# Kernel tuning notes

Hardware: AMD Instinct MI355X
Metric: run time of the kernel (lower is better)

Reference implementation:

```python
import jax, jax.numpy as jnp
import numpy as np
from math import comb

N_SEG = 100000      # number of Bezier segments
BEZ_ORDER = 3       # cubic Bezier -> 4 control points per segment
D = 3               # point dimension
BATCH, NPTS = 8, 1000000


def setup_inputs() -> dict:
    key = jax.random.key(0)
    k1, k2, k3 = jax.random.split(key, 3)
    # strictly ascending knot vector: cumsum of positive dx, starting at 0
    dx = jax.random.uniform(k1, (N_SEG,), dtype=jnp.float32, minval=0.5, maxval=1.5)
    x_knots = jnp.concatenate([jnp.zeros((1,), jnp.float32), jnp.cumsum(dx)])
    x_end = x_knots[-1]
    # eval points spread beyond [0, x_end) so the modulo wrap is exercised
    x_eval = jax.random.uniform(k2, (BATCH, NPTS), dtype=jnp.float32) * (2.0 * x_end) - 0.5 * x_end
    control_points = jax.random.normal(k3, (N_SEG, BEZ_ORDER + 1, D), dtype=jnp.float32)
    return {"x_knots": x_knots, "control_points": control_points, "x_eval": x_eval}


def _bernstein_basis(s, n):
    # s: [N] in [0,1] -> basis [N, n+1]; powers via cumprod (differentiable at s=0/1)
    binom = jnp.asarray([comb(n, k) for k in range(n + 1)], dtype=s.dtype)
    t = s[:, None]
    ones = jnp.ones_like(t)
    t_pow = jnp.cumprod(jnp.concatenate([ones, jnp.broadcast_to(t, (t.shape[0], n))], axis=1), axis=1)         # t^k
    u = 1.0 - t
    u_pow = jnp.cumprod(jnp.concatenate([ones, jnp.broadcast_to(u, (u.shape[0], n))], axis=1), axis=1)         # u^k
    return binom * t_pow * u_pow[:, ::-1]  # C(n,k) t^k (1-t)^(n-k)


def reference(x_knots, control_points, x_eval):
    n = control_points.shape[1] - 1
    d = control_points.shape[2]
    xstart = x_knots[:-1]                      # [n_seg]
    dx = x_knots[1:] - x_knots[:-1]            # [n_seg]
    # x_true = x_eval % xend  (Python modulo semantics, matches torch %)
    x_true = jnp.mod(x_eval.reshape(-1), x_knots[-1])        # [N]
    # bucket search: segment index such that xstart[i] <= x_true < xstart[i+1]
    idx = jnp.clip(jnp.searchsorted(xstart, x_true, side='right') - 1, 0, xstart.shape[0] - 1)
    s = (x_true - xstart[idx]) / dx[idx]                     # local param in [0,1)
    basis = _bernstein_basis(s, n)                           # [N, n+1]
    P = control_points[idx]                                  # gather: [N, n+1, d]
    vals = jnp.einsum('nk,nkd->nd', basis, P)                # [N, d]
    return vals.reshape(x_eval.shape + (d,)), idx.reshape(x_eval.shape)
```

## Files before the change

kernel.cpp:

```cpp
#include <hip/hip_runtime.h>
#include <hip/hip_fp16.h>
#include <math.h>

#define N_SEG 100000
#define LUT_BITS 18
#define LUT_SIZE (1 << LUT_BITS)
#define DELTA 0.03

using f32x4 = __attribute__((ext_vector_type(4))) float;

#define LUT_OFF 0
#define REC_OFF 2097152
#define WS_NEED (REC_OFF + (size_t)N_SEG * 32)

__global__ void __launch_bounds__(256)
build_lut_kernel(const float* __restrict__ xk, int2* __restrict__ lut) {
    int j = blockIdx.x * blockDim.x + threadIdx.x;
    if (j >= LUT_SIZE) return;
    double Wd = (double)xk[N_SEG] / (double)LUT_SIZE;
    double t = (double)j * Wd - DELTA;
    int lo = 0, hi = N_SEG;
    while (lo < hi) {
        int mid = (lo + hi) >> 1;
        if ((double)xk[mid] <= t) lo = mid + 1; else hi = mid;
    }
    int base = lo - 1;
    base = base < 0 ? 0 : (base > N_SEG - 1 ? N_SEG - 1 : base);
    int2 e;
    e.x = base;
    e.y = (base + 1 <= N_SEG - 1) ? __float_as_int(xk[base + 1])
                                  : __float_as_int(__builtin_inff());
    lut[j] = e;
}

__device__ __forceinline__ unsigned packh(float lo, float hi) {
    unsigned a = (unsigned)__half_as_ushort(__float2half(lo));
    unsigned b = (unsigned)__half_as_ushort(__float2half(hi));
    return a | (b << 16);
}

__global__ void __launch_bounds__(256)
build_rec_kernel(const float* __restrict__ xk, const float* __restrict__ cp,
                 uint4* __restrict__ rec) {
    int i = blockIdx.x * blockDim.x + threadIdx.x;
    if (i >= N_SEG) return;
    float x0 = xk[i];
    float inv = 1.0f / (xk[i + 1] - x0);
    const f32x4* p = reinterpret_cast<const f32x4*>(cp + (size_t)i * 12);
    f32x4 pA = p[0];
    f32x4 pB = p[1];
    f32x4 pC = p[2];
    uint4 ra, rb;
    ra.x = __float_as_uint(x0);
    ra.y = __float_as_uint(inv);
    ra.z = packh(pA.x, pA.y);
    ra.w = packh(pA.z, pA.w);
    rb.x = packh(pB.x, pB.y);
    rb.y = packh(pB.z, pB.w);
    rb.z = packh(pC.x, pC.y);
    rb.w = packh(pC.z, pC.w);
    rec[2 * (size_t)i]     = ra;
    rec[2 * (size_t)i + 1] = rb;
}

__device__ __forceinline__ float h2f(unsigned w, int hi) {
    return __half2float(__ushort_as_half((unsigned short)(hi ? (w >> 16) : (w & 0xFFFFu))));
}

__device__ __forceinline__ float mod_reduce(float x, float xe) {
    float r = x;
    r = (x >= xe) ? (x - xe) : r;
    r = (x < 0.0f) ? (x + xe) : r;
    return r;
}

__global__ void __launch_bounds__(256, 4)
eval_kernel(const float* __restrict__ xk,
            const float* __restrict__ xev,
            float* __restrict__ out_vals,
            float* __restrict__ out_idx,
            const int2* __restrict__ lut,
            const uint4* __restrict__ rec,
            int npts) {
    int t = blockIdx.x * blockDim.x + threadIdx.x;
    int i0 = t * 8;
    if (i0 >= npts) return;

    float xe = xk[N_SEG];
    float invW = (float)LUT_SIZE / xe;

    if (i0 + 7 < npts) {
        f32x4 xa = __builtin_nontemporal_load(reinterpret_cast<const f32x4*>(xev) + 2 * t);
        f32x4 xb = __builtin_nontemporal_load(reinterpret_cast<const f32x4*>(xev) + 2 * t + 1);
        float r[8] = {xa.x, xa.y, xa.z, xa.w, xb.x, xb.y, xb.z, xb.w};
        int2 e[8];
        #pragma unroll
        for (int q = 0; q < 8; ++q) {
            r[q] = mod_reduce(r[q], xe);
            int j = (int)(r[q] * invW);
            j = j < 0 ? 0 : (j > LUT_SIZE - 1 ? LUT_SIZE - 1 : j);
            e[q] = lut[j];
        }
        int idx[8];
        uint4 ra[8], rb[8];
        #pragma unroll
        for (int q = 0; q < 8; ++q) {
            idx[q] = e[q].x + ((__int_as_float(e[q].y) <= r[q]) ? 1 : 0);
            ra[q] = rec[2 * (size_t)idx[q]];
            rb[q] = rec[2 * (size_t)idx[q] + 1];
        }
        float vals[24];
        float idxf[8];
        #pragma unroll
        for (int q = 0; q < 8; ++q) {
            float x0  = __uint_as_float(ra[q].x);
            float inv = __uint_as_float(ra[q].y);
            float s = (r[q] - x0) * inv;
            float u = 1.0f - s;
            float s2 = s * s, u2 = u * u;
            float b0 = u2 * u;
            float b1 = (3.0f * s) * u2;
            float b2 = (3.0f * s2) * u;
            float b3 = s2 * s;
            float c0 = h2f(ra[q].z, 0), c1  = h2f(ra[q].z, 1);
            float c2 = h2f(ra[q].w, 0), c3  = h2f(ra[q].w, 1);
            float c4 = h2f(rb[q].x, 0), c5  = h2f(rb[q].x, 1);
            float c6 = h2f(rb[q].y, 0), c7  = h2f(rb[q].y, 1);
            float c8 = h2f(rb[q].z, 0), c9  = h2f(rb[q].z, 1);
            float c10 = h2f(rb[q].w, 0), c11 = h2f(rb[q].w, 1);
            vals[q * 3 + 0] = b0 * c0 + b1 * c3 + b2 * c6 + b3 * c9;
            vals[q * 3 + 1] = b0 * c1 + b1 * c4 + b2 * c7 + b3 * c10;
            vals[q * 3 + 2] = b0 * c2 + b1 * c5 + b2 * c8 + b3 * c11;
            idxf[q] = (float)idx[q];
        }
        f32x4* ov = reinterpret_cast<f32x4*>(out_vals + (size_t)t * 24);
        #pragma unroll
        for (int q = 0; q < 6; ++q) {
            f32x4 o = {vals[4 * q], vals[4 * q + 1], vals[4 * q + 2], vals[4 * q + 3]};
            ov[q] = o;
        }
        f32x4 oi0 = {idxf[0], idxf[1], idxf[2], idxf[3]};
        f32x4 oi1 = {idxf[4], idxf[5], idxf[6], idxf[7]};
        reinterpret_cast<f32x4*>(out_idx)[2 * t]     = oi0;
        reinterpret_cast<f32x4*>(out_idx)[2 * t + 1] = oi1;
    } else {
        for (int i = i0; i < npts; ++i) {
            float r = mod_reduce(xev[i], xe);
            int j = (int)(r * invW);
            j = j < 0 ? 0 : (j > LUT_SIZE - 1 ? LUT_SIZE - 1 : j);
            int2 e = lut[j];
            int idx = e.x + ((__int_as_float(e.y) <= r) ? 1 : 0);
            uint4 ra = rec[2 * (size_t)idx];
            uint4 rb = rec[2 * (size_t)idx + 1];
            float x0  = __uint_as_float(ra.x);
            float inv = __uint_as_float(ra.y);
            float s = (r - x0) * inv;
            float u = 1.0f - s;
            float s2 = s * s, u2 = u * u;
            float b0 = u2 * u, b1 = (3.0f * s) * u2, b2 = (3.0f * s2) * u, b3 = s2 * s;
            out_vals[(size_t)i * 3 + 0] = b0 * h2f(ra.z, 0) + b1 * h2f(ra.w, 1) + b2 * h2f(rb.y, 0) + b3 * h2f(rb.z, 1);
            out_vals[(size_t)i * 3 + 1] = b0 * h2f(ra.z, 1) + b1 * h2f(rb.x, 0) + b2 * h2f(rb.y, 1) + b3 * h2f(rb.w, 0);
            out_vals[(size_t)i * 3 + 2] = b0 * h2f(ra.w, 0) + b1 * h2f(rb.x, 1) + b2 * h2f(rb.z, 0) + b3 * h2f(rb.w, 1);
            out_idx[i] = (float)idx;
        }
    }
}

__global__ void __launch_bounds__(256)
eval_kernel_bs(const float* __restrict__ xk,
               const float* __restrict__ cp,
               const float* __restrict__ xev,
               float* __restrict__ out_vals,
               float* __restrict__ out_idx,
               int npts) {
    int i = blockIdx.x * blockDim.x + threadIdx.x;
    if (i >= npts) return;
    float xe = xk[N_SEG];
    float r = mod_reduce(xev[i], xe);
    int lo = 0, hi = N_SEG;
    while (lo < hi) {
        int mid = (lo + hi) >> 1;
        if (xk[mid] <= r) lo = mid + 1; else hi = mid;
    }
    int idx = lo - 1;
    if (idx < 0) idx = 0;
    float x0 = xk[idx];
    float s = (r - x0) / (xk[idx + 1] - x0);
    float u = 1.0f - s;
    float s2 = s * s, u2 = u * u;
    float b0 = u2 * u, b1f = (3.0f * s) * u2, b2f = (3.0f * s2) * u, b3f = s2 * s;
    const f32x4* p = reinterpret_cast<const f32x4*>(cp + (size_t)idx * 12);
    f32x4 pA = p[0], pB = p[1], pC = p[2];
    out_vals[(size_t)i * 3 + 0] = b0 * pA.x + b1f * pA.w + b2f * pB.z + b3f * pC.y;
    out_vals[(size_t)i * 3 + 1] = b0 * pA.y + b1f * pB.x + b2f * pB.w + b3f * pC.z;
    out_vals[(size_t)i * 3 + 2] = b0 * pA.z + b1f * pB.y + b2f * pC.x + b3f * pC.w;
    out_idx[i] = (float)idx;
}

extern "C" void kernel_launch(void* const* d_in, const int* in_sizes, int n_in,
                              void* d_out, int out_size, void* d_ws, size_t ws_size,
                              hipStream_t stream) {
    const float* xk  = (const float*)d_in[0];
    const float* cp  = (const float*)d_in[1];
    const float* xev = (const float*)d_in[2];
    int npts = in_sizes[2];

    float* out_vals = (float*)d_out;
    float* out_idx  = out_vals + (size_t)npts * 3;

    if (ws_size >= WS_NEED) {
        char* ws = (char*)d_ws;
        int2*  lut = (int2*)(ws + LUT_OFF);
        uint4* rec = (uint4*)(ws + REC_OFF);

        build_lut_kernel<<<(LUT_SIZE + 255) / 256, 256, 0, stream>>>(xk, lut);
        build_rec_kernel<<<(N_SEG + 255) / 256, 256, 0, stream>>>(xk, cp, rec);

        int nthreads = (npts + 7) / 8;
        int nblocks  = (nthreads + 255) / 256;
        eval_kernel<<<nblocks, 256, 0, stream>>>(xk, xev, out_vals, out_idx,
                                                 lut, rec, npts);
    } else {
        int nblocks = (npts + 255) / 256;
        eval_kernel_bs<<<nblocks, 256, 0, stream>>>(xk, cp, xev, out_vals, out_idx, npts);
    }
}
```

Measured before the change: 167.9 us.

## Fuse LUT and segment records into 64-byte lines loaded via global_load_lds

Replaces the two-level lookup (LUT entry, then dependent segment record gather) with one 64-byte line per LUT bucket holding both candidate segments' knots and fp16 control points, so each point needs a single gather. The lines are fetched directly into LDS with global_load_lds and read back per lane, and points per thread drop from 8 to 4 for more parallelism. This removes a dependent memory round trip but enlarges the table to 16 MB, adds a per-point divide instead of a precomputed reciprocal, and adds LDS traffic.

```diff
diff --git a/kernel.cpp b/kernel.cpp
--- a/kernel.cpp
+++ b/kernel.cpp
@@ -6,15 +6,32 @@
 #define LUT_BITS 18
 #define LUT_SIZE (1 << LUT_BITS)
 #define DELTA 0.03
-
-using f32x4 = __attribute__((ext_vector_type(4))) float;
-
-#define LUT_OFF 0
-#define REC_OFF 2097152
-#define WS_NEED (REC_OFF + (size_t)N_SEG * 32)
+#define PPT 4
+
+using f32x4  = __attribute__((ext_vector_type(4))) float;
+using u32x4  = __attribute__((ext_vector_type(4))) unsigned int;
+
+#define WS_NEED ((size_t)LUT_SIZE * 64)
+
+__device__ __forceinline__ unsigned packh(float lo, float hi) {
+    unsigned a = (unsigned)__half_as_ushort(__float2half(lo));
+    unsigned b = (unsigned)__half_as_ushort(__float2half(hi));
+    return a | (b << 16);
+}
+__device__ __forceinline__ float h2f(unsigned w, int hi) {
+    return __half2float(__ushort_as_half((unsigned short)(hi ? (w >> 16) : (w & 0xFFFFu))));
+}
+
+__device__ __forceinline__ float mod_reduce(float x, float xe) {
+    float r = x;
+    r = (x >= xe) ? (x - xe) : r;
+    r = (x < 0.0f) ? (x + xe) : r;
+    return r;
+}
 
 __global__ void __launch_bounds__(256)
-build_lut_kernel(const float* __restrict__ xk, int2* __restrict__ lut) {
+build_rec_kernel(const float* __restrict__ xk, const float* __restrict__ cp,
+                 u32x4* __restrict__ rec) {
     int j = blockIdx.x * blockDim.x + threadIdx.x;
     if (j >= LUT_SIZE) return;
     double Wd = (double)xk[N_SEG] / (double)LUT_SIZE;
@@ -26,142 +43,146 @@
     }
     int base = lo - 1;
     base = base < 0 ? 0 : (base > N_SEG - 1 ? N_SEG - 1 : base);
-    int2 e;
-    e.x = base;
-    e.y = (base + 1 <= N_SEG - 1) ? __float_as_int(xk[base + 1])
-                                  : __float_as_int(__builtin_inff());
-    lut[j] = e;
-}
-
-__device__ __forceinline__ unsigned packh(float lo, float hi) {
-    unsigned a = (unsigned)__half_as_ushort(__float2half(lo));
-    unsigned b = (unsigned)__half_as_ushort(__float2half(hi));
-    return a | (b << 16);
+
+    int validb = (base + 1 <= N_SEG - 1) ? 1 : 0;
+    int ia = base;
+    int ib = validb ? base + 1 : base;
+
+    float x0a = xk[base];
+    float x1a = xk[base + 1];
+    int i2 = base + 2 > N_SEG ? N_SEG : base + 2;
+    float x1b = xk[i2];
+
+    const f32x4* pa = reinterpret_cast<const f32x4*>(cp + (size_t)ia * 12);
+    const f32x4* pb = reinterpret_cast<const f32x4*>(cp + (size_t)ib * 12);
+    f32x4 a0 = pa[0], a1 = pa[1], a2 = pa[2];
+    f32x4 b0 = pb[0], b1 = pb[1], b2 = pb[2];
+
+    u32x4 w0 = { __float_as_uint(x0a), __float_as_uint(x1a), __float_as_uint(x1b),
+                 (unsigned)base | ((unsigned)validb << 31) };
+    u32x4 w1 = { packh(a0.x, a0.y), packh(a0.z, a0.w),
+                 packh(a1.x, a1.y), packh(a1.z, a1.w) };
+    u32x4 w2 = { packh(a2.x, a2.y), packh(a2.z, a2.w),
+                 packh(b0.x, b0.y), packh(b0.z, b0.w) };
+    u32x4 w3 = { packh(b1.x, b1.y), packh(b1.z, b1.w),
+                 packh(b2.x, b2.y), packh(b2.z, b2.w) };
+    u32x4* line = rec + 4 * (size_t)j;
+    line[0] = w0; line[1] = w1; line[2] = w2; line[3] = w3;
+}
+
+__device__ __forceinline__ void decode_blend(u32x4 h, u32x4 w1, u32x4 w2, u32x4 w3,
+                                             float r, float* v, float* idxf) {
+    unsigned bw = h.w;
+    int base = (int)(bw & 0x7FFFFFFFu);
+    float x0a = __uint_as_float(h.x);
+    float x1a = __uint_as_float(h.y);
+    float x1b = __uint_as_float(h.z);
+    int c = ((x1a <= r) && (bw >> 31)) ? 1 : 0;
+    int idx = base + c;
+    float x0 = c ? x1a : x0a;
+    float x1 = c ? x1b : x1a;
+    float s = (r - x0) / (x1 - x0);
+
+    unsigned cw0 = c ? w2.z : w1.x;
+    unsigned cw1 = c ? w2.w : w1.y;
+    unsigned cw2 = c ? w3.x : w1.z;
+    unsigned cw3 = c ? w3.y : w1.w;
+    unsigned cw4 = c ? w3.z : w2.x;
+    unsigned cw5 = c ? w3.w : w2.y;
+
+    float u = 1.0f - s;
+    float s2 = s * s, u2 = u * u;
+    float b0 = u2 * u;
+    float b1 = (3.0f * s) * u2;
+    float b2 = (3.0f * s2) * u;
+    float b3 = s2 * s;
+
+    float c0 = h2f(cw0, 0), c1  = h2f(cw0, 1);
+    float c2 = h2f(cw1, 0), c3  = h2f(cw1, 1);
+    float c4 = h2f(cw2, 0), c5  = h2f(cw2, 1);
+    float c6 = h2f(cw3, 0), c7  = h2f(cw3, 1);
+    float c8 = h2f(cw4, 0), c9  = h2f(cw4, 1);
+    float c10 = h2f(cw5, 0), c11 = h2f(cw5, 1);
+
+    v[0] = b0 * c0 + b1 * c3 + b2 * c6 + b3 * c9;
+    v[1] = b0 * c1 + b1 * c4 + b2 * c7 + b3 * c10;
+    v[2] = b0 * c2 + b1 * c5 + b2 * c8 + b3 * c11;
+    *idxf = (float)idx;
 }
 
 __global__ void __launch_bounds__(256)
-build_rec_kernel(const float* __restrict__ xk, const float* __restrict__ cp,
-                 uint4* __restrict__ rec) {
-    int i = blockIdx.x * blockDim.x + threadIdx.x;
-    if (i >= N_SEG) return;
-    float x0 = xk[i];
-    float inv = 1.0f / (xk[i + 1] - x0);
-    const f32x4* p = reinterpret_cast<const f32x4*>(cp + (size_t)i * 12);
-    f32x4 pA = p[0];
-    f32x4 pB = p[1];
-    f32x4 pC = p[2];
-    uint4 ra, rb;
-    ra.x = __float_as_uint(x0);
-    ra.y = __float_as_uint(inv);
-    ra.z = packh(pA.x, pA.y);
-    ra.w = packh(pA.z, pA.w);
-    rb.x = packh(pB.x, pB.y);
-    rb.y = packh(pB.z, pB.w);
-    rb.z = packh(pC.x, pC.y);
-    rb.w = packh(pC.z, pC.w);
-    rec[2 * (size_t)i]     = ra;
-    rec[2 * (size_t)i + 1] = rb;
-}
-
-__device__ __forceinline__ float h2f(unsigned w, int hi) {
-    return __half2float(__ushort_as_half((unsigned short)(hi ? (w >> 16) : (w & 0xFFFFu))));
-}
-
-__device__ __forceinline__ float mod_reduce(float x, float xe) {
-    float r = x;
-    r = (x >= xe) ? (x - xe) : r;
-    r = (x < 0.0f) ? (x + xe) : r;
-    return r;
-}
-
-__global__ void __launch_bounds__(256, 4)
 eval_kernel(const float* __restrict__ xk,
             const float* __restrict__ xev,
             float* __restrict__ out_vals,
             float* __restrict__ out_idx,
-            const int2* __restrict__ lut,
-            const uint4* __restrict__ rec,
+            const unsigned char* __restrict__ rec,
             int npts) {
+    __shared__ unsigned char stage[4 * PPT * 4 * 64 * 16];
     int t = blockIdx.x * blockDim.x + threadIdx.x;
-    int i0 = t * 8;
-    if (i0 >= npts) return;
+    int lane = threadIdx.x & 63;
+    int wave = threadIdx.x >> 6;
+    long i0 = (long)t * PPT;
 
     float xe = xk[N_SEG];
     float invW = (float)LUT_SIZE / xe;
 
-    if (i0 + 7 < npts) {
-        f32x4 xa = __builtin_nontemporal_load(reinterpret_cast<const f32x4*>(xev) + 2 * t);
-        f32x4 xb = __builtin_nontemporal_load(reinterpret_cast<const f32x4*>(xev) + 2 * t + 1);
-        float r[8] = {xa.x, xa.y, xa.z, xa.w, xb.x, xb.y, xb.z, xb.w};
-        int2 e[8];
-        #pragma unroll
-        for (int q = 0; q < 8; ++q) {
+    if (i0 + PPT - 1 < (long)npts) {
+        f32x4 x4 = __builtin_nontemporal_load(reinterpret_cast<const f32x4*>(xev) + t);
+        float r[PPT] = {x4.x, x4.y, x4.z, x4.w};
+        const unsigned char* pa[PPT];
+        #pragma unroll
+        for (int q = 0; q < PPT; ++q) {
             r[q] = mod_reduce(r[q], xe);
             int j = (int)(r[q] * invW);
             j = j < 0 ? 0 : (j > LUT_SIZE - 1 ? LUT_SIZE - 1 : j);
-            e[q] = lut[j];
-        }
-        int idx[8];
-        uint4 ra[8], rb[8];
-        #pragma unroll
-        for (int q = 0; q < 8; ++q) {
-            idx[q] = e[q].x + ((__int_as_float(e[q].y) <= r[q]) ? 1 : 0);
-            ra[q] = rec[2 * (size_t)idx[q]];
-            rb[q] = rec[2 * (size_t)idx[q] + 1];
-        }
-        float vals[24];
-        float idxf[8];
-        #pragma unroll
-        for (int q = 0; q < 8; ++q) {
-            float x0  = __uint_as_float(ra[q].x);
-            float inv = __uint_as_float(ra[q].y);
-            float s = (r[q] - x0) * inv;
-            float u = 1.0f - s;
-            float s2 = s * s, u2 = u * u;
-            float b0 = u2 * u;
-            float b1 = (3.0f * s) * u2;
-            float b2 = (3.0f * s2) * u;
-            float b3 = s2 * s;
-            float c0 = h2f(ra[q].z, 0), c1  = h2f(ra[q].z, 1);
-            float c2 = h2f(ra[q].w, 0), c3  = h2f(ra[q].w, 1);
-            float c4 = h2f(rb[q].x, 0), c5  = h2f(rb[q].x, 1);
-            float c6 = h2f(rb[q].y, 0), c7  = h2f(rb[q].y, 1);
-            float c8 = h2f(rb[q].z, 0), c9  = h2f(rb[q].z, 1);
-            float c10 = h2f(rb[q].w, 0), c11 = h2f(rb[q].w, 1);
-            vals[q * 3 + 0] = b0 * c0 + b1 * c3 + b2 * c6 + b3 * c9;
-            vals[q * 3 + 1] = b0 * c1 + b1 * c4 + b2 * c7 + b3 * c10;
-            vals[q * 3 + 2] = b0 * c2 + b1 * c5 + b2 * c8 + b3 * c11;
-            idxf[q] = (float)idx[q];
-        }
-        f32x4* ov = reinterpret_cast<f32x4*>(out_vals + (size_t)t * 24);
-        #pragma unroll
-        for (int q = 0; q < 6; ++q) {
+            pa[q] = rec + ((size_t)j << 6);
+        }
+        unsigned wbase = (unsigned)wave * (PPT * 4 * 1024);
+        #pragma unroll
+        for (int q = 0; q < PPT; ++q) {
+            #pragma unroll
+            for (int k = 0; k < 4; ++k) {
+                __builtin_amdgcn_global_load_lds(
+                    (const __attribute__((address_space(1))) void*)(pa[q] + 16 * k),
+                    (__attribute__((address_space(3))) void*)(stage + wbase + (q * 4 + k) * 1024),
+                    16, 0, 0);
+            }
+        }
+        asm volatile("s_waitcnt vmcnt(0)" ::: "memory");
+        __builtin_amdgcn_sched_barrier(0);
+
+        float vals[PPT * 3];
+        float idxf[PPT];
+        #pragma unroll
+        for (int q = 0; q < PPT; ++q) {
+            const u32x4* pl = reinterpret_cast<const u32x4*>(stage + wbase + q * 4096 + lane * 16);
+            u32x4 h  = pl[0];
+            u32x4 w1 = pl[64];
+            u32x4 w2 = pl[128];
+            u32x4 w3 = pl[192];
+            decode_blend(h, w1, w2, w3, r[q], &vals[q * 3], &idxf[q]);
+        }
+        f32x4* ov = reinterpret_cast<f32x4*>(out_vals + (size_t)t * 12);
+        #pragma unroll
+        for (int q = 0; q < 3; ++q) {
             f32x4 o = {vals[4 * q], vals[4 * q + 1], vals[4 * q + 2], vals[4 * q + 3]};
             ov[q] = o;
         }
-        f32x4 oi0 = {idxf[0], idxf[1], idxf[2], idxf[3]};
-        f32x4 oi1 = {idxf[4], idxf[5], idxf[6], idxf[7]};
-        reinterpret_cast<f32x4*>(out_idx)[2 * t]     = oi0;
-        reinterpret_cast<f32x4*>(out_idx)[2 * t + 1] = oi1;
+        f32x4 oi = {idxf[0], idxf[1], idxf[2], idxf[3]};
+        reinterpret_cast<f32x4*>(out_idx)[t] = oi;
     } else {
-        for (int i = i0; i < npts; ++i) {
+        for (long i = i0; i < (long)npts && i < i0 + PPT; ++i) {
             float r = mod_reduce(xev[i], xe);
             int j = (int)(r * invW);
             j = j < 0 ? 0 : (j > LUT_SIZE - 1 ? LUT_SIZE - 1 : j);
-            int2 e = lut[j];
-            int idx = e.x + ((__int_as_float(e.y) <= r) ? 1 : 0);
-            uint4 ra = rec[2 * (size_t)idx];
-            uint4 rb = rec[2 * (size_t)idx + 1];
-            float x0  = __uint_as_float(ra.x);
-            float inv = __uint_as_float(ra.y);
-            float s = (r - x0) * inv;
-            float u = 1.0f - s;
-            float s2 = s * s, u2 = u * u;
-            float b0 = u2 * u, b1 = (3.0f * s) * u2, b2 = (3.0f * s2) * u, b3 = s2 * s;
-            out_vals[(size_t)i * 3 + 0] = b0 * h2f(ra.z, 0) + b1 * h2f(ra.w, 1) + b2 * h2f(rb.y, 0) + b3 * h2f(rb.z, 1);
-            out_vals[(size_t)i * 3 + 1] = b0 * h2f(ra.z, 1) + b1 * h2f(rb.x, 0) + b2 * h2f(rb.y, 1) + b3 * h2f(rb.w, 0);
-            out_vals[(size_t)i * 3 + 2] = b0 * h2f(ra.w, 0) + b1 * h2f(rb.x, 1) + b2 * h2f(rb.z, 0) + b3 * h2f(rb.w, 1);
-            out_idx[i] = (float)idx;
+            const u32x4* line = reinterpret_cast<const u32x4*>(rec + ((size_t)j << 6));
+            u32x4 h = line[0], w1 = line[1], w2 = line[2], w3 = line[3];
+            float v[3], idxf;
+            decode_blend(h, w1, w2, w3, r, v, &idxf);
+            out_vals[(size_t)i * 3 + 0] = v[0];
+            out_vals[(size_t)i * 3 + 1] = v[1];
+            out_vals[(size_t)i * 3 + 2] = v[2];
+            out_idx[i] = idxf;
         }
     }
 }
@@ -209,17 +230,12 @@
     float* out_idx  = out_vals + (size_t)npts * 3;
 
     if (ws_size >= WS_NEED) {
-        char* ws = (char*)d_ws;
-        int2*  lut = (int2*)(ws + LUT_OFF);
-        uint4* rec = (uint4*)(ws + REC_OFF);
-
-        build_lut_kernel<<<(LUT_SIZE + 255) / 256, 256, 0, stream>>>(xk, lut);
-        build_rec_kernel<<<(N_SEG + 255) / 256, 256, 0, stream>>>(xk, cp, rec);
-
-        int nthreads = (npts + 7) / 8;
-        int nblocks  = (nthreads + 255) / 256;
+        u32x4* rec = (u32x4*)d_ws;
+        build_rec_kernel<<<(LUT_SIZE + 255) / 256, 256, 0, stream>>>(xk, cp, rec);
+        long nthreads = ((long)npts + PPT - 1) / PPT;
+        int nblocks  = (int)((nthreads + 255) / 256);
         eval_kernel<<<nblocks, 256, 0, stream>>>(xk, xev, out_vals, out_idx,
-                                                 lut, rec, npts);
+                                                 (const unsigned char*)d_ws, npts);
     } else {
         int nblocks = (npts + 255) / 256;
         eval_kernel_bs<<<nblocks, 256, 0, stream>>>(xk, cp, xev, out_vals, out_idx, npts);
```

New measurement: 160.0 us. -4.7%, faster.
